# Performance work log

Measured on AMD Instinct MI355X. Metric: run time of the kernel, lower is better.

The kernel has to match this reference:

```python
import jax, jax.numpy as jnp
import numpy as np

N_NODES = 10242  # icosphere level-5 node count
NNZ = 71694      # ~7 nonzeros per row (6 neighbors + self)


def setup_inputs() -> dict:
    key = jax.random.key(0)
    k1, k2, k3, k4, k5 = jax.random.split(key, 5)
    B, T, C, Cout, Ks = 2, 16, 16, 32, 20
    x = jax.random.normal(k1, (B, T, N_NODES, C), dtype=jnp.float32)
    edge_row = jax.random.randint(k2, (NNZ,), 0, N_NODES, dtype=jnp.int32)
    edge_col = jax.random.randint(k3, (NNZ,), 0, N_NODES, dtype=jnp.int32)
    # small values keep the Chebyshev recurrence numerically bounded over Ks steps
    edge_val = jax.random.uniform(k4, (NNZ,), dtype=jnp.float32, minval=-0.2, maxval=0.2)
    W = jax.random.normal(k5, (Cout, C * Ks), dtype=jnp.float32) * 0.02
    return {"x": x, "edge_row": edge_row, "edge_col": edge_col,
            "edge_val": edge_val, "W": W}


def reference(x, edge_row, edge_col, edge_val, W):
    B, T, N, C = x.shape
    Cout, CK = W.shape
    Ks = CK // C

    def spmm(v):  # sparse L @ v, v: [N, F]
        return jax.ops.segment_sum(edge_val[:, None] * v[edge_col], edge_row,
                                   num_segments=N)

    # [B,T,N,C] -> [B*T,N,C] -> [N,C,B*T] -> [N, C*B*T]
    x0 = x.reshape(B * T, N, C).transpose(1, 2, 0).reshape(N, C * B * T)
    x1 = spmm(x0)

    def step(carry, _):
        a, b = carry
        c = 2.0 * spmm(b) - a
        return (b, c), c

    _, rest = jax.lax.scan(step, (x0, x1), None, length=Ks - 2)
    xs = jnp.concatenate([x0[None], x1[None], rest], axis=0)  # [Ks, N, C*B*T]

    xs = xs.reshape(Ks, N, C, B * T).transpose(3, 1, 2, 0)  # [B*T, N, C, Ks]
    xs = xs.reshape(B * T * N, C * Ks)
    out = xs @ W.T  # [B*T*N, Cout]
    return out.reshape(B, T, N, Cout)
```

## Files before the change

### kernel.cpp

```cpp
#include <hip/hip_runtime.h>

#define N_NODES 10242
#define NNZ_E   71694
#define NNZ_PAD_MAX (NNZ_E + 7 * N_NODES + 64)
#define BT      32
#define C_IN    16
#define K_S     20
#define C_OUT   32
#define F       512
typedef unsigned short u16;
typedef unsigned int   u32;

#define RING_ELEMS ((size_t)N_NODES * F)
#define RING_BYTES (RING_ELEMS * 2)

typedef __attribute__((ext_vector_type(8)))  _Float16 half8;
typedef __attribute__((ext_vector_type(16))) float    float16;

__device__ __forceinline__ void unpack8h(uint4 u, float* f) {
    union { uint4 u; _Float16 h[8]; } v; v.u = u;
    #pragma unroll
    for (int i = 0; i < 8; ++i) f[i] = (float)v.h[i];
}
__device__ __forceinline__ uint4 pack8h(const float* f) {
    union { uint4 u; _Float16 h[8]; } v;
    #pragma unroll
    for (int i = 0; i < 8; ++i) v.h[i] = (_Float16)f[i];
    return v.u;
}
__device__ __forceinline__ u16 f2h(float f) {
    union { _Float16 h; u16 u; } v; v.h = (_Float16)f; return v.u;
}


__global__ __launch_bounds__(256) void init_kernel(
        const float* __restrict__ W, int* __restrict__ cnt,
        u16* __restrict__ wtfrag) {
    int i = blockIdx.x * 256 + threadIdx.x;
    if (i < N_NODES) cnt[i] = 0;
    int w = i - N_NODES;
    if (w >= 0 && w < K_S * 64 * 8) {
        int j    = w & 7;
        int lane = (w >> 3) & 63;
        int k    = w >> 9;
        int cout = lane & 31;
        int c    = ((lane >> 5) << 3) + j;
        wtfrag[w] = f2h(W[cout * (C_IN * K_S) + c * K_S + k]);
    }
}

__global__ __launch_bounds__(256) void count_kernel(
        const int* __restrict__ erow, int* cnt) {
    int e = blockIdx.x * 256 + threadIdx.x;
    if (e < NNZ_E) atomicAdd(&cnt[erow[e]], 1);
}

__global__ __launch_bounds__(256) void scan_kernel(
        const int* __restrict__ cnt, int* row_ptr, int* cursor) {
    const int T = 256;
    const int chunk = (N_NODES + T - 1) / T;
    __shared__ int part[T];
    int t = threadIdx.x;
    int base = t * chunk;
    int s = 0;
    for (int i = 0; i < chunk; ++i) {
        int idx = base + i;
        if (idx < N_NODES) s += (cnt[idx] + 7) & ~7;
    }
    part[t] = s;
    __syncthreads();
    for (int off = 1; off < T; off <<= 1) {
        int v = (t >= off) ? part[t - off] : 0;
        __syncthreads();
        part[t] += v;
        __syncthreads();
    }
    int run = (t == 0) ? 0 : part[t - 1];
    for (int i = 0; i < chunk; ++i) {
        int idx = base + i;
        if (idx < N_NODES) {
            row_ptr[idx] = run;
            cursor[idx]  = run;
            run += (cnt[idx] + 7) & ~7;
        }
    }
    if (t == T - 1) row_ptr[N_NODES] = part[T - 1];
}

__global__ __launch_bounds__(256) void scatter_kernel(
        const int* __restrict__ erow, const int* __restrict__ ecol,
        const float* __restrict__ eval, int* cursor, int2* __restrict__ cpack) {
    int e = blockIdx.x * 256 + threadIdx.x;
    if (e < NNZ_E) {
        int p = atomicAdd(&cursor[erow[e]], 1);
        cpack[p] = make_int2(ecol[e], __float_as_int(eval[e]));
    }
}

__global__ __launch_bounds__(256) void finalize_kernel(
        const int* __restrict__ row_ptr, const int* __restrict__ cursor,
        int2* cpack) {
    int r = blockIdx.x * 256 + threadIdx.x;
    if (r >= N_NODES) return;
    int sbeg = row_ptr[r];
    int send = cursor[r];
    int pend = row_ptr[r + 1];
    for (int i = sbeg + 1; i < send; ++i) {
        int2 key = cpack[i];
        int j = i - 1;
        while (j >= sbeg) {
            int2 q = cpack[j];
            bool gt = (q.x > key.x) || (q.x == key.x && (u32)q.y > (u32)key.y);
            if (!gt) break;
            cpack[j + 1] = q;
            --j;
        }
        cpack[j + 1] = key;
    }
    for (int p = send; p < pend; ++p) cpack[p] = make_int2(0, 0);
}


__global__ __launch_bounds__(256) void transform_kernel(
        const float* __restrict__ x, u16* __restrict__ T0) {
    int g = blockIdx.x * 256 + threadIdx.x;
    int n   = g >> 9;
    int rem = g & 511;
    int bt  = rem >> 4;
    int c   = rem & 15;
    float v = x[((size_t)bt * N_NODES + n) * C_IN + c];
    T0[(size_t)n * F + rem] = f2h(v);
}


__global__ __launch_bounds__(256) void spmm_step_kernel(
        const u16* __restrict__ srcB, const u16* __restrict__ srcA,
        u16* __restrict__ dst,
        const int* __restrict__ row_ptr, const int2* __restrict__ cpack,
        float alpha, float beta) {
    const int lane = threadIdx.x & 63;
    const int n = (blockIdx.x << 2) + (threadIdx.x >> 6);
    if (n >= N_NODES) return;
    const int s = row_ptr[n], e_end = row_ptr[n + 1];

    float a[8] = {0,0,0,0,0,0,0,0};
    if (beta != 0.f) {
        uint4 ua = ((const uint4*)(srcA + (size_t)n * F))[lane];
        unpack8h(ua, a);
    }

    int2 my = cpack[s + lane];

    float acc0[8] = {0,0,0,0,0,0,0,0};
    float acc1[8] = {0,0,0,0,0,0,0,0};

    for (int e = s; e < e_end; e += 8) {
        const int base = e - s;
        int c0 = __builtin_amdgcn_readlane(my.x, base + 0);
        int c1 = __builtin_amdgcn_readlane(my.x, base + 1);
        int c2 = __builtin_amdgcn_readlane(my.x, base + 2);
        int c3 = __builtin_amdgcn_readlane(my.x, base + 3);
        int c4 = __builtin_amdgcn_readlane(my.x, base + 4);
        int c5 = __builtin_amdgcn_readlane(my.x, base + 5);
        int c6 = __builtin_amdgcn_readlane(my.x, base + 6);
        int c7 = __builtin_amdgcn_readlane(my.x, base + 7);
        float v0 = __int_as_float(__builtin_amdgcn_readlane(my.y, base + 0));
        float v1 = __int_as_float(__builtin_amdgcn_readlane(my.y, base + 1));
        float v2 = __int_as_float(__builtin_amdgcn_readlane(my.y, base + 2));
        float v3 = __int_as_float(__builtin_amdgcn_readlane(my.y, base + 3));
        float v4 = __int_as_float(__builtin_amdgcn_readlane(my.y, base + 4));
        float v5 = __int_as_float(__builtin_amdgcn_readlane(my.y, base + 5));
        float v6 = __int_as_float(__builtin_amdgcn_readlane(my.y, base + 6));
        float v7 = __int_as_float(__builtin_amdgcn_readlane(my.y, base + 7));

        uint4 g0 = ((const uint4*)(srcB + (size_t)c0 * F))[lane];
        uint4 g1 = ((const uint4*)(srcB + (size_t)c1 * F))[lane];
        uint4 g2 = ((const uint4*)(srcB + (size_t)c2 * F))[lane];
        uint4 g3 = ((const uint4*)(srcB + (size_t)c3 * F))[lane];
        uint4 g4 = ((const uint4*)(srcB + (size_t)c4 * F))[lane];
        uint4 g5 = ((const uint4*)(srcB + (size_t)c5 * F))[lane];
        uint4 g6 = ((const uint4*)(srcB + (size_t)c6 * F))[lane];
        uint4 g7 = ((const uint4*)(srcB + (size_t)c7 * F))[lane];

        float b0[8], b1[8], b2[8], b3[8], b4[8], b5[8], b6[8], b7[8];
        unpack8h(g0, b0); unpack8h(g1, b1); unpack8h(g2, b2); unpack8h(g3, b3);
        unpack8h(g4, b4); unpack8h(g5, b5); unpack8h(g6, b6); unpack8h(g7, b7);

        #pragma unroll
        for (int i = 0; i < 8; ++i) {
            acc0[i] += v0 * b0[i];
            acc1[i] += v1 * b1[i];
            acc0[i] += v2 * b2[i];
            acc1[i] += v3 * b3[i];
            acc0[i] += v4 * b4[i];
            acc1[i] += v5 * b5[i];
            acc0[i] += v6 * b6[i];
            acc1[i] += v7 * b7[i];
        }
    }

    float y[8];
    #pragma unroll
    for (int i = 0; i < 8; ++i)
        y[i] = alpha * (acc0[i] + acc1[i]) + beta * a[i];

    ((uint4*)(dst + (size_t)n * F))[lane] = pack8h(y);
}


__global__ __launch_bounds__(256) void proj_mfma_kernel(
        const u16* __restrict__ ring, int R, int k0, int kcnt,
        const u16* __restrict__ wtfrag, float* __restrict__ out, int accumulate) {
    const int lane = threadIdx.x & 63;
    const int n = (blockIdx.x << 2) + (threadIdx.x >> 6);
    if (n >= N_NODES) return;
    const int col = lane & 31;
    const int grp = lane >> 5;
    const size_t aoff = (size_t)n * F + (size_t)col * 16 + grp * 8;

    union U { uint4 u; half8 h; };
    float16 acc0 = {};
    float16 acc1 = {};
    int j = 0;
    for (; j + 2 <= kcnt; j += 2) {
        int ka = k0 + j, kb = k0 + j + 1;
        U a0, b0, a1, b1;
        a0.u = *(const uint4*)(ring + (size_t)(ka % R) * RING_ELEMS + aoff);
        b0.u = *(const uint4*)(wtfrag + (size_t)ka * 512 + lane * 8);
        a1.u = *(const uint4*)(ring + (size_t)(kb % R) * RING_ELEMS + aoff);
        b1.u = *(const uint4*)(wtfrag + (size_t)kb * 512 + lane * 8);
        acc0 = __builtin_amdgcn_mfma_f32_32x32x16_f16(a0.h, b0.h, acc0, 0, 0, 0);
        acc1 = __builtin_amdgcn_mfma_f32_32x32x16_f16(a1.h, b1.h, acc1, 0, 0, 0);
    }
    if (j < kcnt) {
        int ka = k0 + j;
        U a0, b0;
        a0.u = *(const uint4*)(ring + (size_t)(ka % R) * RING_ELEMS + aoff);
        b0.u = *(const uint4*)(wtfrag + (size_t)ka * 512 + lane * 8);
        acc0 = __builtin_amdgcn_mfma_f32_32x32x16_f16(a0.h, b0.h, acc0, 0, 0, 0);
    }

    #pragma unroll
    for (int r = 0; r < 16; ++r) {
        int bt = (r & 3) + 8 * (r >> 2) + 4 * grp;
        float* op = out + ((size_t)bt * N_NODES + n) * C_OUT + col;
        float val = acc0[r] + acc1[r];
        if (accumulate) *op += val;
        else            *op  = val;
    }
}


extern "C" void kernel_launch(void* const* d_in, const int* in_sizes, int n_in,
                              void* d_out, int out_size, void* d_ws, size_t ws_size,
                              hipStream_t stream) {
    const float* x    = (const float*)d_in[0];
    const int*   erow = (const int*)  d_in[1];
    const int*   ecol = (const int*)  d_in[2];
    const float* eval = (const float*)d_in[3];
    const float* W    = (const float*)d_in[4];
    float* out = (float*)d_out;

    char* ws = (char*)d_ws;
    size_t o = 0;
    auto alloc = [&](size_t bytes) -> char* {
        o = (o + 511) & ~(size_t)511;
        char* r = ws + o;
        o += bytes;
        return r;
    };
    int*   cnt     = (int*)  alloc((size_t)N_NODES * 4);
    int*   row_ptr = (int*)  alloc((size_t)(N_NODES + 1) * 4);
    int*   cursor  = (int*)  alloc((size_t)N_NODES * 4);
    int2*  cpack   = (int2*) alloc((size_t)NNZ_PAD_MAX * 8);
    u16*   wtfrag  = (u16*)  alloc((size_t)K_S * 512 * 2);

    o = (o + 511) & ~(size_t)511;
    int R = (int)((ws_size - o) / RING_BYTES);
    if (R > K_S) R = K_S;
    if (R < 3)  R = 3;
    u16* ring = (u16*)(ws + o);
    auto slot = [&](int k) -> u16* { return ring + (size_t)(k % R) * RING_ELEMS; };

    init_kernel<<<(N_NODES + K_S * 512 + 255) / 256, 256, 0, stream>>>(W, cnt, wtfrag);
    count_kernel<<<(NNZ_E + 255) / 256, 256, 0, stream>>>(erow, cnt);
    scan_kernel<<<1, 256, 0, stream>>>(cnt, row_ptr, cursor);
    scatter_kernel<<<(NNZ_E + 255) / 256, 256, 0, stream>>>(erow, ecol, eval, cursor, cpack);
    finalize_kernel<<<(N_NODES + 255) / 256, 256, 0, stream>>>(row_ptr, cursor, cpack);

    const int grid4 = (N_NODES + 3) / 4;
    int c0 = 0;
    auto maybe_pass = [&](int k_done) {
        int target = K_S - c0;
        if (target > R) target = R;
        if (target > 0 && (k_done - c0 + 1) == target) {
            proj_mfma_kernel<<<grid4, 256, 0, stream>>>(
                ring, R, c0, target, wtfrag, out, (c0 > 0) ? 1 : 0);
            c0 += target;
        }
    };

    transform_kernel<<<(int)(RING_ELEMS / 256), 256, 0, stream>>>(x, slot(0));
    maybe_pass(0);

    for (int k = 1; k < K_S; ++k) {
        const u16* srcB = slot(k - 1);
        const u16* srcA = (k >= 2) ? slot(k - 2) : slot(k - 1);
        float alpha = (k == 1) ? 1.f : 2.f;
        float beta  = (k == 1) ? 0.f : -1.f;
        spmm_step_kernel<<<grid4, 256, 0, stream>>>(
            srcB, srcA, slot(k), row_ptr, cpack, alpha, beta);
        maybe_pass(k);
    }
}
```

Baseline: 456.5 us.

## Fuse Chebyshev recurrence and projection into one cooperative persistent kernel

```diff
diff --git a/kernel.cpp b/kernel.cpp
--- a/kernel.cpp
+++ b/kernel.cpp
@@ -1,4 +1,7 @@
 #include <hip/hip_runtime.h>
+#include <hip/hip_cooperative_groups.h>
+
+namespace cg = cooperative_groups;
 
 #define N_NODES 10242
 #define NNZ_E   71694
@@ -13,6 +16,10 @@
 
 #define RING_ELEMS ((size_t)N_NODES * F)
 #define RING_BYTES (RING_ELEMS * 2)
+
+#define NBLK_F   256
+#define TPB_F    1024
+#define NWAVES_F (NBLK_F * (TPB_F / 64))
 
 typedef __attribute__((ext_vector_type(8)))  _Float16 half8;
 typedef __attribute__((ext_vector_type(16))) float    float16;
@@ -121,57 +128,64 @@
 }
 
 
-__global__ __launch_bounds__(256) void transform_kernel(
-        const float* __restrict__ x, u16* __restrict__ T0) {
-    int g = blockIdx.x * 256 + threadIdx.x;
-    int n   = g >> 9;
-    int rem = g & 511;
-    int bt  = rem >> 4;
-    int c   = rem & 15;
-    float v = x[((size_t)bt * N_NODES + n) * C_IN + c];
-    T0[(size_t)n * F + rem] = f2h(v);
-}
-
-
-__global__ __launch_bounds__(256) void spmm_step_kernel(
+__device__ __forceinline__ void mfma_step(float16& acc, uint4 yp,
+                                          const u16* __restrict__ wfk, int lane) {
+    int S = ((lane & 31) << 1) | (lane >> 5);
+    uint4 af;
+    af.x = (u32)__shfl((int)yp.x, S, 64);
+    af.y = (u32)__shfl((int)yp.y, S, 64);
+    af.z = (u32)__shfl((int)yp.z, S, 64);
+    af.w = (u32)__shfl((int)yp.w, S, 64);
+    union { uint4 u; half8 h; } au, bu;
+    au.u = af;
+    bu.u = *(const uint4*)(wfk + lane * 8);
+    acc = __builtin_amdgcn_mfma_f32_32x32x16_f16(au.h, bu.h, acc, 0, 0, 0);
+}
+
+__device__ __forceinline__ void xform_node(int n, int lane,
+        const float* __restrict__ x, u16* __restrict__ dst0,
+        const u16* __restrict__ wf0, float16& acc) {
+    int bt = lane >> 1;
+    int hc = (lane & 1) * 8;
+    const float* xp = x + ((size_t)bt * N_NODES + n) * C_IN + hc;
+    float4 f0 = *(const float4*)xp;
+    float4 f1 = *(const float4*)(xp + 4);
+    float y[8] = {f0.x, f0.y, f0.z, f0.w, f1.x, f1.y, f1.z, f1.w};
+    uint4 yp = pack8h(y);
+    ((uint4*)(dst0 + (size_t)n * F))[lane] = yp;
+    mfma_step(acc, yp, wf0, lane);
+}
+
+__device__ __forceinline__ void step_node(int n, int len, int2 my, int lane,
         const u16* __restrict__ srcB, const u16* __restrict__ srcA,
-        u16* __restrict__ dst,
-        const int* __restrict__ row_ptr, const int2* __restrict__ cpack,
-        float alpha, float beta) {
-    const int lane = threadIdx.x & 63;
-    const int n = (blockIdx.x << 2) + (threadIdx.x >> 6);
-    if (n >= N_NODES) return;
-    const int s = row_ptr[n], e_end = row_ptr[n + 1];
-
+        u16* __restrict__ dst, float alpha, float beta,
+        const u16* __restrict__ wfk, float16& acc) {
     float a[8] = {0,0,0,0,0,0,0,0};
     if (beta != 0.f) {
         uint4 ua = ((const uint4*)(srcA + (size_t)n * F))[lane];
         unpack8h(ua, a);
     }
 
-    int2 my = cpack[s + lane];
-
     float acc0[8] = {0,0,0,0,0,0,0,0};
     float acc1[8] = {0,0,0,0,0,0,0,0};
 
-    for (int e = s; e < e_end; e += 8) {
-        const int base = e - s;
-        int c0 = __builtin_amdgcn_readlane(my.x, base + 0);
-        int c1 = __builtin_amdgcn_readlane(my.x, base + 1);
-        int c2 = __builtin_amdgcn_readlane(my.x, base + 2);
-        int c3 = __builtin_amdgcn_readlane(my.x, base + 3);
-        int c4 = __builtin_amdgcn_readlane(my.x, base + 4);
-        int c5 = __builtin_amdgcn_readlane(my.x, base + 5);
-        int c6 = __builtin_amdgcn_readlane(my.x, base + 6);
-        int c7 = __builtin_amdgcn_readlane(my.x, base + 7);
-        float v0 = __int_as_float(__builtin_amdgcn_readlane(my.y, base + 0));
-        float v1 = __int_as_float(__builtin_amdgcn_readlane(my.y, base + 1));
-        float v2 = __int_as_float(__builtin_amdgcn_readlane(my.y, base + 2));
-        float v3 = __int_as_float(__builtin_amdgcn_readlane(my.y, base + 3));
-        float v4 = __int_as_float(__builtin_amdgcn_readlane(my.y, base + 4));
-        float v5 = __int_as_float(__builtin_amdgcn_readlane(my.y, base + 5));
-        float v6 = __int_as_float(__builtin_amdgcn_readlane(my.y, base + 6));
-        float v7 = __int_as_float(__builtin_amdgcn_readlane(my.y, base + 7));
+    for (int e = 0; e < len; e += 8) {
+        int c0 = __builtin_amdgcn_readlane(my.x, e + 0);
+        int c1 = __builtin_amdgcn_readlane(my.x, e + 1);
+        int c2 = __builtin_amdgcn_readlane(my.x, e + 2);
+        int c3 = __builtin_amdgcn_readlane(my.x, e + 3);
+        int c4 = __builtin_amdgcn_readlane(my.x, e + 4);
+        int c5 = __builtin_amdgcn_readlane(my.x, e + 5);
+        int c6 = __builtin_amdgcn_readlane(my.x, e + 6);
+        int c7 = __builtin_amdgcn_readlane(my.x, e + 7);
+        float v0 = __int_as_float(__builtin_amdgcn_readlane(my.y, e + 0));
+        float v1 = __int_as_float(__builtin_amdgcn_readlane(my.y, e + 1));
+        float v2 = __int_as_float(__builtin_amdgcn_readlane(my.y, e + 2));
+        float v3 = __int_as_float(__builtin_amdgcn_readlane(my.y, e + 3));
+        float v4 = __int_as_float(__builtin_amdgcn_readlane(my.y, e + 4));
+        float v5 = __int_as_float(__builtin_amdgcn_readlane(my.y, e + 5));
+        float v6 = __int_as_float(__builtin_amdgcn_readlane(my.y, e + 6));
+        float v7 = __int_as_float(__builtin_amdgcn_readlane(my.y, e + 7));
 
         uint4 g0 = ((const uint4*)(srcB + (size_t)c0 * F))[lane];
         uint4 g1 = ((const uint4*)(srcB + (size_t)c1 * F))[lane];
@@ -204,9 +218,147 @@
     for (int i = 0; i < 8; ++i)
         y[i] = alpha * (acc0[i] + acc1[i]) + beta * a[i];
 
+    uint4 yp = pack8h(y);
+    ((uint4*)(dst + (size_t)n * F))[lane] = yp;
+    mfma_step(acc, yp, wfk, lane);
+}
+
+__device__ __forceinline__ void write_out(int n, int lane, const float16& acc,
+                                          float* __restrict__ out) {
+    int col = lane & 31;
+    int grp = lane >> 5;
+    #pragma unroll
+    for (int r = 0; r < 16; ++r) {
+        int bt = (r & 3) + 8 * (r >> 2) + 4 * grp;
+        out[((size_t)bt * N_NODES + n) * C_OUT + col] = acc[r];
+    }
+}
+
+__global__ __launch_bounds__(1024, 4) void cheb_fused_kernel(
+        const float* __restrict__ x,
+        const int* __restrict__ row_ptr, const int2* __restrict__ cpack,
+        const u16* __restrict__ wtfrag, u16* __restrict__ ring,
+        float* __restrict__ out) {
+    cg::grid_group grid = cg::this_grid();
+    const int lane = threadIdx.x & 63;
+    const int wid  = blockIdx.x * (TPB_F / 64) + (threadIdx.x >> 6);
+
+    const int n0 = wid;
+    const int n1 = wid + NWAVES_F;
+    const int n2 = wid + 2 * NWAVES_F;
+    const bool v2 = (n2 < N_NODES);
+
+    int  l0 = row_ptr[n0 + 1] - row_ptr[n0];
+    int  l1 = row_ptr[n1 + 1] - row_ptr[n1];
+    int  l2 = v2 ? (row_ptr[n2 + 1] - row_ptr[n2]) : 0;
+    int2 my0 = cpack[row_ptr[n0] + lane];
+    int2 my1 = cpack[row_ptr[n1] + lane];
+    int2 my2 = v2 ? cpack[row_ptr[n2] + lane] : make_int2(0, 0);
+
+    float16 ac0 = {}, ac1 = {}, ac2 = {};
+
+    xform_node(n0, lane, x, ring, wtfrag, ac0);
+    xform_node(n1, lane, x, ring, wtfrag, ac1);
+    if (v2) xform_node(n2, lane, x, ring, wtfrag, ac2);
+    grid.sync();
+
+    for (int k = 1; k < K_S; ++k) {
+        const u16* srcB = ring + (size_t)((k - 1) % 3) * RING_ELEMS;
+        const u16* srcA = ring + (size_t)((k + 1) % 3) * RING_ELEMS;
+        u16*       dst  = ring + (size_t)(k % 3) * RING_ELEMS;
+        float alpha = (k == 1) ? 1.f : 2.f;
+        float beta  = (k == 1) ? 0.f : -1.f;
+        const u16* wfk = wtfrag + (size_t)k * 512;
+
+        step_node(n0, l0, my0, lane, srcB, srcA, dst, alpha, beta, wfk, ac0);
+        step_node(n1, l1, my1, lane, srcB, srcA, dst, alpha, beta, wfk, ac1);
+        if (v2) step_node(n2, l2, my2, lane, srcB, srcA, dst, alpha, beta, wfk, ac2);
+        grid.sync();
+    }
+
+    write_out(n0, lane, ac0, out);
+    write_out(n1, lane, ac1, out);
+    if (v2) write_out(n2, lane, ac2, out);
+}
+
+
+__global__ __launch_bounds__(256) void transform_kernel(
+        const float* __restrict__ x, u16* __restrict__ T0) {
+    int g = blockIdx.x * 256 + threadIdx.x;
+    int n   = g >> 9;
+    int rem = g & 511;
+    int bt  = rem >> 4;
+    int c   = rem & 15;
+    float v = x[((size_t)bt * N_NODES + n) * C_IN + c];
+    T0[(size_t)n * F + rem] = f2h(v);
+}
+
+__global__ __launch_bounds__(256) void spmm_step_kernel(
+        const u16* __restrict__ srcB, const u16* __restrict__ srcA,
+        u16* __restrict__ dst,
+        const int* __restrict__ row_ptr, const int2* __restrict__ cpack,
+        float alpha, float beta) {
+    const int lane = threadIdx.x & 63;
+    const int n = (blockIdx.x << 2) + (threadIdx.x >> 6);
+    if (n >= N_NODES) return;
+    const int s = row_ptr[n];
+    const int len = row_ptr[n + 1] - s;
+    int2 my = cpack[s + lane];
+    float16 dummy = {};
+    (void)dummy;
+    float a[8] = {0,0,0,0,0,0,0,0};
+    if (beta != 0.f) {
+        uint4 ua = ((const uint4*)(srcA + (size_t)n * F))[lane];
+        unpack8h(ua, a);
+    }
+    float acc0[8] = {0,0,0,0,0,0,0,0};
+    float acc1[8] = {0,0,0,0,0,0,0,0};
+    for (int e = 0; e < len; e += 8) {
+        int c0 = __builtin_amdgcn_readlane(my.x, e + 0);
+        int c1 = __builtin_amdgcn_readlane(my.x, e + 1);
+        int c2 = __builtin_amdgcn_readlane(my.x, e + 2);
+        int c3 = __builtin_amdgcn_readlane(my.x, e + 3);
+        int c4 = __builtin_amdgcn_readlane(my.x, e + 4);
+        int c5 = __builtin_amdgcn_readlane(my.x, e + 5);
+        int c6 = __builtin_amdgcn_readlane(my.x, e + 6);
+        int c7 = __builtin_amdgcn_readlane(my.x, e + 7);
+        float v0 = __int_as_float(__builtin_amdgcn_readlane(my.y, e + 0));
+        float v1 = __int_as_float(__builtin_amdgcn_readlane(my.y, e + 1));
+        float v2 = __int_as_float(__builtin_amdgcn_readlane(my.y, e + 2));
+        float v3 = __int_as_float(__builtin_amdgcn_readlane(my.y, e + 3));
+        float v4 = __int_as_float(__builtin_amdgcn_readlane(my.y, e + 4));
+        float v5 = __int_as_float(__builtin_amdgcn_readlane(my.y, e + 5));
+        float v6 = __int_as_float(__builtin_amdgcn_readlane(my.y, e + 6));
+        float v7 = __int_as_float(__builtin_amdgcn_readlane(my.y, e + 7));
+        uint4 g0 = ((const uint4*)(srcB + (size_t)c0 * F))[lane];
+        uint4 g1 = ((const uint4*)(srcB + (size_t)c1 * F))[lane];
+        uint4 g2 = ((const uint4*)(srcB + (size_t)c2 * F))[lane];
+        uint4 g3 = ((const uint4*)(srcB + (size_t)c3 * F))[lane];
+        uint4 g4 = ((const uint4*)(srcB + (size_t)c4 * F))[lane];
+        uint4 g5 = ((const uint4*)(srcB + (size_t)c5 * F))[lane];
+        uint4 g6 = ((const uint4*)(srcB + (size_t)c6 * F))[lane];
+        uint4 g7 = ((const uint4*)(srcB + (size_t)c7 * F))[lane];
+        float b0[8], b1[8], b2[8], b3[8], b4[8], b5[8], b6[8], b7[8];
+        unpack8h(g0, b0); unpack8h(g1, b1); unpack8h(g2, b2); unpack8h(g3, b3);
+        unpack8h(g4, b4); unpack8h(g5, b5); unpack8h(g6, b6); unpack8h(g7, b7);
+        #pragma unroll
+        for (int i = 0; i < 8; ++i) {
+            acc0[i] += v0 * b0[i];
+            acc1[i] += v1 * b1[i];
+            acc0[i] += v2 * b2[i];
+            acc1[i] += v3 * b3[i];
+            acc0[i] += v4 * b4[i];
+            acc1[i] += v5 * b5[i];
+            acc0[i] += v6 * b6[i];
+            acc1[i] += v7 * b7[i];
+        }
+    }
+    float y[8];
+    #pragma unroll
+    for (int i = 0; i < 8; ++i)
+        y[i] = alpha * (acc0[i] + acc1[i]) + beta * a[i];
     ((uint4*)(dst + (size_t)n * F))[lane] = pack8h(y);
 }
-
 
 __global__ __launch_bounds__(256) void proj_mfma_kernel(
         const u16* __restrict__ ring, int R, int k0, int kcnt,
@@ -217,7 +369,6 @@
     const int col = lane & 31;
     const int grp = lane >> 5;
     const size_t aoff = (size_t)n * F + (size_t)col * 16 + grp * 8;
-
     union U { uint4 u; half8 h; };
     float16 acc0 = {};
     float16 acc1 = {};
@@ -239,7 +390,6 @@
         b0.u = *(const uint4*)(wtfrag + (size_t)ka * 512 + lane * 8);
         acc0 = __builtin_amdgcn_mfma_f32_32x32x16_f16(a0.h, b0.h, acc0, 0, 0, 0);
     }
-
     #pragma unroll
     for (int r = 0; r < 16; ++r) {
         int bt = (r & 3) + 8 * (r >> 2) + 4 * grp;
@@ -288,6 +438,18 @@
     scatter_kernel<<<(NNZ_E + 255) / 256, 256, 0, stream>>>(erow, ecol, eval, cursor, cpack);
     finalize_kernel<<<(N_NODES + 255) / 256, 256, 0, stream>>>(row_ptr, cursor, cpack);
 
+    {
+        const float* xa = x; const int* rpa = row_ptr; const int2* cpa = cpack;
+        const u16* wfa = wtfrag; u16* ra = ring; float* oa = out;
+        void* args[] = {(void*)&xa, (void*)&rpa, (void*)&cpa,
+                        (void*)&wfa, (void*)&ra, (void*)&oa};
+        hipError_t err = hipLaunchCooperativeKernel(
+            (const void*)cheb_fused_kernel, dim3(NBLK_F), dim3(TPB_F),
+            args, 0, stream);
+        if (err == hipSuccess) return;
+        (void)hipGetLastError();
+    }
+
     const int grid4 = (N_NODES + 3) / 4;
     int c0 = 0;
     auto maybe_pass = [&](int k_done) {
@@ -302,7 +464,6 @@
 
     transform_kernel<<<(int)(RING_ELEMS / 256), 256, 0, stream>>>(x, slot(0));
     maybe_pass(0);
-
     for (int k = 1; k < K_S; ++k) {
         const u16* srcB = slot(k - 1);
         const u16* srcA = (k >= 2) ? slot(k - 2) : slot(k - 1);
```

New measurement: 1.313 ms. +187.7%, slower.

## Split SpMM feature dimension into slices with eight rows per wave

Applied to the files above, without the earlier changes.

```diff
diff --git a/kernel.cpp b/kernel.cpp
--- a/kernel.cpp
+++ b/kernel.cpp
@@ -13,6 +13,9 @@
 
 #define RING_ELEMS ((size_t)N_NODES * F)
 #define RING_BYTES (RING_ELEMS * 2)
+
+#define NSLICE  8
+#define SLICE_U16 (F / NSLICE)
 
 typedef __attribute__((ext_vector_type(8)))  _Float16 half8;
 typedef __attribute__((ext_vector_type(16))) float    float16;
@@ -133,78 +136,72 @@
 }
 
 
-__global__ __launch_bounds__(256) void spmm_step_kernel(
+__global__ __launch_bounds__(256) void spmm_slice_kernel(
         const u16* __restrict__ srcB, const u16* __restrict__ srcA,
         u16* __restrict__ dst,
         const int* __restrict__ row_ptr, const int2* __restrict__ cpack,
         float alpha, float beta) {
-    const int lane = threadIdx.x & 63;
-    const int n = (blockIdx.x << 2) + (threadIdx.x >> 6);
-    if (n >= N_NODES) return;
-    const int s = row_ptr[n], e_end = row_ptr[n + 1];
+    const int slice = blockIdx.x & 7;
+    const int chunk = blockIdx.x >> 3;
+    const int wave  = threadIdx.x >> 6;
+    const int lane  = threadIdx.x & 63;
+    const int l     = lane & 7;
+    const int n     = chunk * 32 + wave * 8 + (lane >> 3);
+    const bool valid = (n < N_NODES);
+
+    const int s   = valid ? row_ptr[n] : 0;
+    const int len = valid ? (row_ptr[n + 1] - s) : 0;
+
+    const size_t soff = (size_t)slice * SLICE_U16 + (size_t)l * 8;
 
     float a[8] = {0,0,0,0,0,0,0,0};
-    if (beta != 0.f) {
-        uint4 ua = ((const uint4*)(srcA + (size_t)n * F))[lane];
+    if (beta != 0.f && valid) {
+        uint4 ua = *(const uint4*)(srcA + (size_t)n * F + soff);
         unpack8h(ua, a);
     }
 
-    int2 my = cpack[s + lane];
-
-    float acc0[8] = {0,0,0,0,0,0,0,0};
-    float acc1[8] = {0,0,0,0,0,0,0,0};
-
-    for (int e = s; e < e_end; e += 8) {
-        const int base = e - s;
-        int c0 = __builtin_amdgcn_readlane(my.x, base + 0);
-        int c1 = __builtin_amdgcn_readlane(my.x, base + 1);
-        int c2 = __builtin_amdgcn_readlane(my.x, base + 2);
-        int c3 = __builtin_amdgcn_readlane(my.x, base + 3);
-        int c4 = __builtin_amdgcn_readlane(my.x, base + 4);
-        int c5 = __builtin_amdgcn_readlane(my.x, base + 5);
-        int c6 = __builtin_amdgcn_readlane(my.x, base + 6);
-        int c7 = __builtin_amdgcn_readlane(my.x, base + 7);
-        float v0 = __int_as_float(__builtin_amdgcn_readlane(my.y, base + 0));
-        float v1 = __int_as_float(__builtin_amdgcn_readlane(my.y, base + 1));
-        float v2 = __int_as_float(__builtin_amdgcn_readlane(my.y, base + 2));
-        float v3 = __int_as_float(__builtin_amdgcn_readlane(my.y, base + 3));
-        float v4 = __int_as_float(__builtin_amdgcn_readlane(my.y, base + 4));
-        float v5 = __int_as_float(__builtin_amdgcn_readlane(my.y, base + 5));
-        float v6 = __int_as_float(__builtin_amdgcn_readlane(my.y, base + 6));
-        float v7 = __int_as_float(__builtin_amdgcn_readlane(my.y, base + 7));
-
-        uint4 g0 = ((const uint4*)(srcB + (size_t)c0 * F))[lane];
-        uint4 g1 = ((const uint4*)(srcB + (size_t)c1 * F))[lane];
-        uint4 g2 = ((const uint4*)(srcB + (size_t)c2 * F))[lane];
-        uint4 g3 = ((const uint4*)(srcB + (size_t)c3 * F))[lane];
-        uint4 g4 = ((const uint4*)(srcB + (size_t)c4 * F))[lane];
-        uint4 g5 = ((const uint4*)(srcB + (size_t)c5 * F))[lane];
-        uint4 g6 = ((const uint4*)(srcB + (size_t)c6 * F))[lane];
-        uint4 g7 = ((const uint4*)(srcB + (size_t)c7 * F))[lane];
-
+    float acc[8] = {0,0,0,0,0,0,0,0};
+    const int gbase = lane & 56;
+
+    for (int c = 0; c * 8 < len; ++c) {
+        int2 my = cpack[s + c * 8 + l];
+        int col[8]; float v[8];
+        #pragma unroll
+        for (int r = 0; r < 8; ++r) {
+            col[r] = __shfl(my.x, gbase + r, 64);
+            v[r]   = __int_as_float(__shfl(my.y, gbase + r, 64));
+        }
+        uint4 g0 = *(const uint4*)(srcB + (size_t)col[0] * F + soff);
+        uint4 g1 = *(const uint4*)(srcB + (size_t)col[1] * F + soff);
+        uint4 g2 = *(const uint4*)(srcB + (size_t)col[2] * F + soff);
+        uint4 g3 = *(const uint4*)(srcB + (size_t)col[3] * F + soff);
+        uint4 g4 = *(const uint4*)(srcB + (size_t)col[4] * F + soff);
+        uint4 g5 = *(const uint4*)(srcB + (size_t)col[5] * F + soff);
+        uint4 g6 = *(const uint4*)(srcB + (size_t)col[6] * F + soff);
+        uint4 g7 = *(const uint4*)(srcB + (size_t)col[7] * F + soff);
         float b0[8], b1[8], b2[8], b3[8], b4[8], b5[8], b6[8], b7[8];
         unpack8h(g0, b0); unpack8h(g1, b1); unpack8h(g2, b2); unpack8h(g3, b3);
         unpack8h(g4, b4); unpack8h(g5, b5); unpack8h(g6, b6); unpack8h(g7, b7);
-
         #pragma unroll
         for (int i = 0; i < 8; ++i) {
-            acc0[i] += v0 * b0[i];
-            acc1[i] += v1 * b1[i];
-            acc0[i] += v2 * b2[i];
-            acc1[i] += v3 * b3[i];
-            acc0[i] += v4 * b4[i];
-            acc1[i] += v5 * b5[i];
-            acc0[i] += v6 * b6[i];
-            acc1[i] += v7 * b7[i];
-        }
-    }
-
-    float y[8];
-    #pragma unroll
-    for (int i = 0; i < 8; ++i)
-        y[i] = alpha * (acc0[i] + acc1[i]) + beta * a[i];
-
-    ((uint4*)(dst + (size_t)n * F))[lane] = pack8h(y);
+            acc[i] += v[0] * b0[i];
+            acc[i] += v[1] * b1[i];
+            acc[i] += v[2] * b2[i];
+            acc[i] += v[3] * b3[i];
+            acc[i] += v[4] * b4[i];
+            acc[i] += v[5] * b5[i];
+            acc[i] += v[6] * b6[i];
+            acc[i] += v[7] * b7[i];
+        }
+    }
+
+    if (valid) {
+        float y[8];
+        #pragma unroll
+        for (int i = 0; i < 8; ++i)
+            y[i] = alpha * acc[i] + beta * a[i];
+        *(uint4*)(dst + (size_t)n * F + soff) = pack8h(y);
+    }
 }
 
 
@@ -288,7 +285,8 @@
     scatter_kernel<<<(NNZ_E + 255) / 256, 256, 0, stream>>>(erow, ecol, eval, cursor, cpack);
     finalize_kernel<<<(N_NODES + 255) / 256, 256, 0, stream>>>(row_ptr, cursor, cpack);
 
-    const int grid4 = (N_NODES + 3) / 4;
+    const int grid4  = (N_NODES + 3) / 4;
+    const int gridsl = NSLICE * ((N_NODES + 31) / 32);
     int c0 = 0;
     auto maybe_pass = [&](int k_done) {
         int target = K_S - c0;
@@ -308,7 +306,7 @@
         const u16* srcA = (k >= 2) ? slot(k - 2) : slot(k - 1);
         float alpha = (k == 1) ? 1.f : 2.f;
         float beta  = (k == 1) ? 0.f : -1.f;
-        spmm_step_kernel<<<grid4, 256, 0, stream>>>(
+        spmm_slice_kernel<<<gridsl, 256, 0, stream>>>(
             srcB, srcA, slot(k), row_ptr, cpack, alpha, beta);
         maybe_pass(k);
     }
```

Measured after the change: 451.0 us. About the same (-1.2%).
